# Kernel tuning notes

Measured on AMD Instinct MI355X. Metric: run time of the kernel, lower is better.

The kernel has to match this reference:

```python
import jax, jax.numpy as jnp
import numpy as np

DIM = 2048
N_HEAD = 16
HEAD_DIM = DIM // N_HEAD


def setup_inputs() -> dict:
    key = jax.random.key(0)
    k1, k2, k3 = jax.random.split(key, 3)
    B, N = 8, 4096
    x = jax.random.normal(k1, (B, N, DIM), dtype=jnp.float32)
    # torch nn.Linear weights: [out_features, in_features]
    w_qkv = jax.random.normal(k2, (3 * DIM, DIM), dtype=jnp.float32) * (DIM ** -0.5)
    w_proj = jax.random.normal(k3, (DIM, DIM), dtype=jnp.float32) * (DIM ** -0.5)
    return {"x": x, "w_qkv": w_qkv, "w_proj": w_proj}


def reference(x, w_qkv, w_proj):
    # Faithful to the original torch code, INCLUDING its layout quirk:
    # q,k,v stay [B, N, H, hd]; attention matrix is [B, N, H, H]
    # (softmax over heads, per token), matching q @ k.transpose(-2, -1).
    B, N, D = x.shape
    H, hd = N_HEAD, HEAD_DIM
    qkv = (x @ w_qkv.T).reshape(B, N, 3, H, hd)
    q, k, v = qkv[:, :, 0], qkv[:, :, 1], qkv[:, :, 2]  # each [B, N, H, hd]
    scale = hd ** -0.5
    att = jnp.einsum("bnid,bnjd->bnij", q, k) * scale  # [B, N, H, H]
    att = jax.nn.softmax(att, axis=-1)
    out = jnp.einsum("bnij,bnjd->bnid", att, v)  # [B, N, H, hd]
    # torch: .transpose(1, 2).reshape(B, N, D)
    out = out.transpose(0, 2, 1, 3).reshape(B, N, D)
    return out @ w_proj.T
```

## Files before the change

### kernel.cpp

```cpp
#include <hip/hip_runtime.h>


typedef unsigned short u16;
typedef unsigned int   u32;
typedef __bf16  bf16x8  __attribute__((ext_vector_type(8)));
typedef float   floatx4 __attribute__((ext_vector_type(4)));

#define GAS __attribute__((address_space(1)))
#define LAS __attribute__((address_space(3)))

__device__ __forceinline__ u16 f2bf(float x) {
  u32 u = __builtin_bit_cast(u32, x);
  return (u16)((u + 0x7FFFu + ((u >> 16) & 1u)) >> 16);
}
__device__ __forceinline__ u32 f2bf2(float lo, float hi) {
  u32 a = __builtin_bit_cast(u32, lo);
  u32 b = __builtin_bit_cast(u32, hi);
  a = (a + 0x7FFFu + ((a >> 16) & 1u)) >> 16;
  b = (b + 0x7FFFu + ((b >> 16) & 1u)) >> 16;
  return a | (b << 16);
}
__device__ __forceinline__ float bf2f(u32 lo16) {
  return __builtin_bit_cast(float, lo16 << 16);
}
__device__ __forceinline__ void unpack8(uint4 r, float* f) {
  f[0] = bf2f(r.x & 0xffffu); f[1] = bf2f(r.x >> 16);
  f[2] = bf2f(r.y & 0xffffu); f[3] = bf2f(r.y >> 16);
  f[4] = bf2f(r.z & 0xffffu); f[5] = bf2f(r.z >> 16);
  f[6] = bf2f(r.w & 0xffffu); f[7] = bf2f(r.w >> 16);
}

__global__ __launch_bounds__(256)
void cast_bf16_k(const float4* __restrict__ in, uint4* __restrict__ out, long n8) {
  long i = (long)blockIdx.x * 256 + threadIdx.x;
  if (i >= n8) return;
  float4 a = in[2 * i], b = in[2 * i + 1];
  uint4 o;
  o.x = f2bf2(a.x, a.y); o.y = f2bf2(a.z, a.w);
  o.z = f2bf2(b.x, b.y); o.w = f2bf2(b.z, b.w);
  out[i] = o;
}

__device__ __forceinline__ void mfma_quad(floatx4 (&acc)[8][4], const bf16x8 (&af)[2][4],
                                          const bf16x8 (&bv)[2][4], int ib, int nb) {
#pragma unroll
  for (int kk = 0; kk < 2; ++kk)
#pragma unroll
    for (int i = 0; i < 4; ++i)
#pragma unroll
      for (int n = 0; n < 2; ++n)
        acc[ib + i][nb + n] = __builtin_amdgcn_mfma_f32_16x16x32_bf16(
            af[kk][i], bv[kk][nb + n], acc[ib + i][nb + n], 0, 0, 0);
}

template<int OUT_BF16>
__global__ __launch_bounds__(512, 2)
void gemm256_k(const u16* __restrict__ A, const u16* __restrict__ B,
               void* __restrict__ Cv, int N_, int K, int nbx)
{
  __shared__ __align__(16) char smem[131072];

  const int nwg = (int)gridDim.x;
  const int id  = (int)blockIdx.x;
  const int swz = (id & 7) * (nwg >> 3) + (id >> 3);
  const int bx = swz % nbx, by = swz / nbx;
  const long tileM = (long)by << 8, tileN = (long)bx << 8;

  const int t = (int)threadIdx.x;
  const int wave = t >> 6, lane = t & 63;
  const int wm = wave >> 2, wn = wave & 3;
  const int lrow = lane & 15, lkq = lane >> 4;

  const int o0   = t << 4;
  const int r0   = (o0 >> 6) & 15;
  const int c0   = (o0 & 63) ^ ((r0 & 8) << 2);
  const int row0 = ((o0 >> 11) << 4) | r0;
  const int col0 = (((o0 >> 10) & 1) << 5) + (c0 >> 1);

  const u16* pA = A + (tileM + row0) * (long)K + col0;
  const u16* pB = B + (tileN + row0) * (long)K + col0;
  const long rs64 = (long)K << 6;
  const int  nkt  = K >> 6;

  const int innerF = (lrow << 6) | ((lkq << 4) ^ ((lrow & 8) << 2));
  const int aB = (wm << 14) + innerF;
  const int bB = 32768 + (wn << 13) + innerF;

  floatx4 acc[8][4] = {};
  bf16x8 af[2][4], bv[2][4];

  auto stage = [&](int s, int j) {
    const int base = ((j & 1) << 16) + ((s < 2) ? 32768 : 0) + ((s & 1) << 14) + (wave << 10);
    const u16* src = (s < 2) ? pB : pA;
    const long gofs = (long)(s & 1) * 2 * rs64 + ((long)j << 6);
    __builtin_amdgcn_global_load_lds((GAS void*)(src + gofs),        (LAS void*)(smem + base),        16, 0, 0);
    __builtin_amdgcn_global_load_lds((GAS void*)(src + gofs + rs64), (LAS void*)(smem + base + 8192), 16, 0, 0);
  };

  stage(0, 0); stage(1, 0); stage(2, 0); stage(3, 0);
  if (nkt > 1) { stage(0, 1); stage(1, 1); stage(2, 1); }
  asm volatile("s_waitcnt vmcnt(6)" ::: "memory");
  __builtin_amdgcn_s_barrier();
  __builtin_amdgcn_sched_barrier(0);

  for (int j = 0; j < nkt; ++j) {
    const int bufo = (j & 1) << 16;

    {
#pragma unroll
      for (int kk = 0; kk < 2; ++kk) {
#pragma unroll
        for (int n = 0; n < 4; ++n)
          bv[kk][n] = *(const bf16x8*)(smem + bufo + bB + (n << 11) + (kk << 10));
#pragma unroll
        for (int i = 0; i < 4; ++i)
          af[kk][i] = *(const bf16x8*)(smem + bufo + aB + (i << 11) + (kk << 10));
      }
      const int h = 4 * j + 7;
      if (h < 4 * nkt) stage(h & 3, h >> 2);
      __builtin_amdgcn_s_barrier();
      asm volatile("s_waitcnt lgkmcnt(0)" ::: "memory");
      __builtin_amdgcn_sched_barrier(0);
      __builtin_amdgcn_s_setprio(1);
      mfma_quad(acc, af, bv, 0, 0);
      __builtin_amdgcn_s_setprio(0);
      __builtin_amdgcn_s_barrier();
      __builtin_amdgcn_sched_barrier(0);
    }
    {
      const int h = 4 * j + 8;
      if (h < 4 * nkt) stage(h & 3, h >> 2);
      __builtin_amdgcn_s_barrier();
      asm volatile("s_waitcnt lgkmcnt(0)" ::: "memory");
      __builtin_amdgcn_sched_barrier(0);
      __builtin_amdgcn_s_setprio(1);
      mfma_quad(acc, af, bv, 0, 2);
      __builtin_amdgcn_s_setprio(0);
      __builtin_amdgcn_s_barrier();
      __builtin_amdgcn_sched_barrier(0);
    }
    {
#pragma unroll
      for (int kk = 0; kk < 2; ++kk)
#pragma unroll
        for (int i = 0; i < 4; ++i)
          af[kk][i] = *(const bf16x8*)(smem + bufo + aB + ((4 + i) << 11) + (kk << 10));
      const int h = 4 * j + 9;
      if (h < 4 * nkt) stage(h & 3, h >> 2);
      __builtin_amdgcn_s_barrier();
      asm volatile("s_waitcnt lgkmcnt(0)" ::: "memory");
      __builtin_amdgcn_sched_barrier(0);
      __builtin_amdgcn_s_setprio(1);
      mfma_quad(acc, af, bv, 4, 0);
      __builtin_amdgcn_s_setprio(0);
      __builtin_amdgcn_s_barrier();
      __builtin_amdgcn_sched_barrier(0);
    }
    {
      const int h = 4 * j + 10;
      if (h < 4 * nkt) stage(h & 3, h >> 2);
      __builtin_amdgcn_s_barrier();
      asm volatile("s_waitcnt lgkmcnt(0)" ::: "memory");
      __builtin_amdgcn_sched_barrier(0);
      __builtin_amdgcn_s_setprio(1);
      mfma_quad(acc, af, bv, 4, 2);
      __builtin_amdgcn_s_setprio(0);
      if (j < nkt - 2)       { asm volatile("s_waitcnt vmcnt(6)" ::: "memory"); }
      else if (j == nkt - 2) { asm volatile("s_waitcnt vmcnt(0)" ::: "memory"); }
      __builtin_amdgcn_s_barrier();
      __builtin_amdgcn_sched_barrier(0);
    }
  }

#pragma unroll
  for (int i = 0; i < 8; ++i) {
#pragma unroll
    for (int r = 0; r < 4; ++r) {
      const long row = tileM + wm * 128 + i * 16 + lkq * 4 + r;
#pragma unroll
      for (int n = 0; n < 4; ++n) {
        const long col = tileN + wn * 64 + n * 16 + lrow;
        const float v = acc[i][n][r];
        if (OUT_BF16) ((u16*)Cv)[row * (long)N_ + col] = f2bf(v);
        else          ((float*)Cv)[row * (long)N_ + col] = v;
      }
    }
  }
}

__global__ __launch_bounds__(256)
void attn_k(const u16* __restrict__ qkv, u16* __restrict__ y)
{
  __shared__ float sq[16 * 132];
  __shared__ float skT[128 * 17];
  __shared__ float sv[16 * 128];
  __shared__ float sS[16 * 17];
  __shared__ float sP[16 * 17];

  const int t = threadIdx.x;
  const int token = blockIdx.x;
  const int n = token & 4095;
  const int b = token >> 12;
  const u16* base = qkv + (long)token * 6144;

  float f[8];
  {
    uint4 raw = *(const uint4*)(base + t * 8);
    unpack8(raw, f);
    float* dst = &sq[(t >> 4) * 132 + (t & 15) * 8];
    ((float4*)dst)[0] = make_float4(f[0], f[1], f[2], f[3]);
    ((float4*)dst)[1] = make_float4(f[4], f[5], f[6], f[7]);
  }
  {
    uint4 raw = *(const uint4*)(base + 2048 + t * 8);
    unpack8(raw, f);
    const int j = t >> 4;
    const int d0 = (t & 15) * 8;
#pragma unroll
    for (int e = 0; e < 8; ++e) skT[(d0 + e) * 17 + j] = f[e];
  }
  {
    uint4 raw = *(const uint4*)(base + 4096 + t * 8);
    unpack8(raw, f);
    float* dst = &sv[t * 8];
    ((float4*)dst)[0] = make_float4(f[0], f[1], f[2], f[3]);
    ((float4*)dst)[1] = make_float4(f[4], f[5], f[6], f[7]);
  }
  __syncthreads();

  {
    const int i = t >> 4, j = t & 15;
    const float* qi = &sq[i * 132];
    float s = 0.f;
#pragma unroll 16
    for (int d = 0; d < 128; ++d) s += qi[d] * skT[d * 17 + j];
    sS[i * 17 + j] = s * 0.08838834764831845f;
  }
  __syncthreads();

  {
    const int i = t >> 4, j = t & 15;
    float mx = -1e30f;
#pragma unroll
    for (int jj = 0; jj < 16; ++jj) mx = fmaxf(mx, sS[i * 17 + jj]);
    float sum = 0.f;
#pragma unroll
    for (int jj = 0; jj < 16; ++jj) sum += __expf(sS[i * 17 + jj] - mx);
    sP[i * 17 + j] = __expf(sS[i * 17 + j] - mx) / sum;
  }
  __syncthreads();

  {
    const int i = t & 15, dblk = t >> 4;
    float o[8] = {};
#pragma unroll
    for (int jj = 0; jj < 16; ++jj) {
      const float p = sP[i * 17 + jj];
      const float* vv = &sv[jj * 128 + dblk * 8];
#pragma unroll
      for (int e = 0; e < 8; ++e) o[e] += p * vv[e];
    }
    const long row  = (long)b * 4096 + i * 256 + (n >> 4);
    const long colb = (long)(n & 15) * 128 + dblk * 8;
    uint4 pk;
    pk.x = f2bf2(o[0], o[1]); pk.y = f2bf2(o[2], o[3]);
    pk.z = f2bf2(o[4], o[5]); pk.w = f2bf2(o[6], o[7]);
    *(uint4*)&y[row * 2048 + colb] = pk;
  }
}

extern "C" void kernel_launch(void* const* d_in, const int* in_sizes, int n_in,
                              void* d_out, int out_size, void* d_ws, size_t ws_size,
                              hipStream_t stream)
{
  const float* x      = (const float*)d_in[0];
  const float* w_qkv  = (const float*)d_in[1];
  const float* w_proj = (const float*)d_in[2];

  const long NX  = 67108864L;
  const long NWQ = 12582912L;
  const long NWP = 4194304L;
  const long NQKV = 32768L * 6144;
  const long NY   = 32768L * 2048;

  char* ws = (char*)d_ws;
  u16* xb   = (u16*)ws;  ws += NX * 2;
  u16* wqb  = (u16*)ws;  ws += NWQ * 2;
  u16* wpb  = (u16*)ws;  ws += NWP * 2;
  u16* qkvb = (u16*)ws;  ws += NQKV * 2;
  u16* yb   = (u16*)ws;  ws += NY * 2;
  if (ws_size < (size_t)704643072L) return;

  cast_bf16_k<<<dim3((u32)(NX  / 2048)), 256, 0, stream>>>((const float4*)x,      (uint4*)xb,  NX  / 8);
  cast_bf16_k<<<dim3((u32)(NWQ / 2048)), 256, 0, stream>>>((const float4*)w_qkv,  (uint4*)wqb, NWQ / 8);
  cast_bf16_k<<<dim3((u32)(NWP / 2048)), 256, 0, stream>>>((const float4*)w_proj, (uint4*)wpb, NWP / 8);

  gemm256_k<1><<<dim3(24 * 128), 512, 0, stream>>>(xb, wqb, (void*)qkvb, 6144, 2048, 24);

  attn_k<<<dim3(32768), 256, 0, stream>>>(qkvb, yb);

  gemm256_k<0><<<dim3(8 * 128), 512, 0, stream>>>(yb, wpb, d_out, 2048, 2048, 8);
}
```

Before: 1.578 ms.

## Restructure GEMM K-loop phases by k-half and batch global prefetch stages

Reorganizes each K-tile iteration into four phases that each cover a full 4x4 MFMA block for one k-half, loading only the LDS fragments needed per phase instead of preloading both k-halves up front. Global-to-LDS staging is regrouped into two pairs per iteration (next tile's stages 2,3 and the tile after's stages 0,1), with vmcnt thresholds adjusted to match. This aims to spread LDS reads across phases and simplify the prefetch schedule, but it changes the prefetch depth and may expose more global-load latency or race on buffer reuse.

Result: faster. 1.542 ms (-2.3%).

```diff
diff --git a/kernel.cpp b/kernel.cpp
--- a/kernel.cpp
+++ b/kernel.cpp
@@ -41,16 +41,15 @@
   out[i] = o;
 }
 
-__device__ __forceinline__ void mfma_quad(floatx4 (&acc)[8][4], const bf16x8 (&af)[2][4],
-                                          const bf16x8 (&bv)[2][4], int ib, int nb) {
-#pragma unroll
-  for (int kk = 0; kk < 2; ++kk)
-#pragma unroll
-    for (int i = 0; i < 4; ++i)
-#pragma unroll
-      for (int n = 0; n < 2; ++n)
-        acc[ib + i][nb + n] = __builtin_amdgcn_mfma_f32_16x16x32_bf16(
-            af[kk][i], bv[kk][nb + n], acc[ib + i][nb + n], 0, 0, 0);
+
+__device__ __forceinline__ void mfma_16(floatx4 (&acc)[8][4], const bf16x8 (&a)[4],
+                                        const bf16x8 (&b)[4], int ib) {
+#pragma unroll
+  for (int i = 0; i < 4; ++i)
+#pragma unroll
+    for (int n = 0; n < 4; ++n)
+      acc[ib + i][n] = __builtin_amdgcn_mfma_f32_16x16x32_bf16(
+          a[i], b[n], acc[ib + i][n], 0, 0, 0);
 }
 
 template<int OUT_BF16>
@@ -98,8 +97,9 @@
   };
 
   stage(0, 0); stage(1, 0); stage(2, 0); stage(3, 0);
-  if (nkt > 1) { stage(0, 1); stage(1, 1); stage(2, 1); }
-  asm volatile("s_waitcnt vmcnt(6)" ::: "memory");
+  if (nkt > 1) { stage(0, 1); stage(1, 1); }
+  if (nkt > 1) { asm volatile("s_waitcnt vmcnt(4)" ::: "memory"); }
+  else         { asm volatile("s_waitcnt vmcnt(0)" ::: "memory"); }
   __builtin_amdgcn_s_barrier();
   __builtin_amdgcn_sched_barrier(0);
 
@@ -108,65 +108,63 @@
 
     {
 #pragma unroll
-      for (int kk = 0; kk < 2; ++kk) {
-#pragma unroll
-        for (int n = 0; n < 4; ++n)
-          bv[kk][n] = *(const bf16x8*)(smem + bufo + bB + (n << 11) + (kk << 10));
-#pragma unroll
-        for (int i = 0; i < 4; ++i)
-          af[kk][i] = *(const bf16x8*)(smem + bufo + aB + (i << 11) + (kk << 10));
-      }
-      const int h = 4 * j + 7;
-      if (h < 4 * nkt) stage(h & 3, h >> 2);
+      for (int n = 0; n < 4; ++n)
+        bv[0][n] = *(const bf16x8*)(smem + bufo + bB + (n << 11));
+#pragma unroll
+      for (int i = 0; i < 4; ++i)
+        af[0][i] = *(const bf16x8*)(smem + bufo + aB + (i << 11));
+      if (j + 1 < nkt) { stage(2, j + 1); stage(3, j + 1); }
       __builtin_amdgcn_s_barrier();
       asm volatile("s_waitcnt lgkmcnt(0)" ::: "memory");
       __builtin_amdgcn_sched_barrier(0);
       __builtin_amdgcn_s_setprio(1);
-      mfma_quad(acc, af, bv, 0, 0);
+      mfma_16(acc, af[0], bv[0], 0);
       __builtin_amdgcn_s_setprio(0);
       __builtin_amdgcn_s_barrier();
       __builtin_amdgcn_sched_barrier(0);
     }
     {
-      const int h = 4 * j + 8;
-      if (h < 4 * nkt) stage(h & 3, h >> 2);
+#pragma unroll
+      for (int n = 0; n < 4; ++n)
+        bv[1][n] = *(const bf16x8*)(smem + bufo + bB + (n << 11) + 1024);
+#pragma unroll
+      for (int i = 0; i < 4; ++i)
+        af[1][i] = *(const bf16x8*)(smem + bufo + aB + (i << 11) + 1024);
       __builtin_amdgcn_s_barrier();
       asm volatile("s_waitcnt lgkmcnt(0)" ::: "memory");
       __builtin_amdgcn_sched_barrier(0);
       __builtin_amdgcn_s_setprio(1);
-      mfma_quad(acc, af, bv, 0, 2);
+      mfma_16(acc, af[1], bv[1], 0);
       __builtin_amdgcn_s_setprio(0);
       __builtin_amdgcn_s_barrier();
       __builtin_amdgcn_sched_barrier(0);
     }
     {
 #pragma unroll
-      for (int kk = 0; kk < 2; ++kk)
-#pragma unroll
-        for (int i = 0; i < 4; ++i)
-          af[kk][i] = *(const bf16x8*)(smem + bufo + aB + ((4 + i) << 11) + (kk << 10));
-      const int h = 4 * j + 9;
-      if (h < 4 * nkt) stage(h & 3, h >> 2);
+      for (int i = 0; i < 4; ++i)
+        af[0][i] = *(const bf16x8*)(smem + bufo + aB + ((4 + i) << 11));
+      if (j + 2 < nkt) { stage(0, j + 2); stage(1, j + 2); }
       __builtin_amdgcn_s_barrier();
       asm volatile("s_waitcnt lgkmcnt(0)" ::: "memory");
       __builtin_amdgcn_sched_barrier(0);
       __builtin_amdgcn_s_setprio(1);
-      mfma_quad(acc, af, bv, 4, 0);
+      mfma_16(acc, af[0], bv[0], 4);
       __builtin_amdgcn_s_setprio(0);
       __builtin_amdgcn_s_barrier();
       __builtin_amdgcn_sched_barrier(0);
     }
     {
-      const int h = 4 * j + 10;
-      if (h < 4 * nkt) stage(h & 3, h >> 2);
+#pragma unroll
+      for (int i = 0; i < 4; ++i)
+        af[1][i] = *(const bf16x8*)(smem + bufo + aB + ((4 + i) << 11) + 1024);
       __builtin_amdgcn_s_barrier();
       asm volatile("s_waitcnt lgkmcnt(0)" ::: "memory");
       __builtin_amdgcn_sched_barrier(0);
       __builtin_amdgcn_s_setprio(1);
-      mfma_quad(acc, af, bv, 4, 2);
+      mfma_16(acc, af[1], bv[1], 4);
       __builtin_amdgcn_s_setprio(0);
-      if (j < nkt - 2)       { asm volatile("s_waitcnt vmcnt(6)" ::: "memory"); }
-      else if (j == nkt - 2) { asm volatile("s_waitcnt vmcnt(0)" ::: "memory"); }
+      if (j < nkt - 2)       { asm volatile("s_waitcnt vmcnt(4)" ::: "memory"); }
+      else                   { asm volatile("s_waitcnt vmcnt(0)" ::: "memory"); }
       __builtin_amdgcn_s_barrier();
       __builtin_amdgcn_sched_barrier(0);
     }
```
